# Performance work log

Hardware: AMD Instinct MI355X
Metric: run time of the kernel (lower is better)

Reference implementation:

```python
import jax, jax.numpy as jnp
import numpy as np

B, T = 64, 4096
NUM_CLASSES = 32000
EMBED_DIM = 128


def setup_inputs() -> dict:
    key = jax.random.key(0)
    k_x, k_w, k_b = jax.random.split(key, 3)
    x = jax.random.randint(k_x, (B, T), 0, NUM_CLASSES, dtype=jnp.int64)
    # torch nn.Linear(num_classes, embed_dim): weight (embed_dim, num_classes), bias (embed_dim,)
    W = jax.random.normal(k_w, (EMBED_DIM, NUM_CLASSES), dtype=jnp.float32) * 0.02
    b = jax.random.normal(k_b, (EMBED_DIM,), dtype=jnp.float32) * 0.02
    return {"x": x, "W": W, "b": b}


def reference(x, W, b):
    # one_hot(x) @ W.T + b  ==  gather rows of W.T at x, plus bias
    # W.T: (num_classes, embed_dim); out: (B, T, embed_dim)
    return jnp.take(W.T, x, axis=0) + b
```

## Files before the change

kernel.cpp:

```cpp
#include <hip/hip_runtime.h>

#define NUM_CLASSES 32000
#define EMBED 128
#define NTOK (64 * 4096)
#define CLS_PER_BLK 64
#define NCHUNK (NUM_CLASSES / CLS_PER_BLK)
#define NREP 16
#define SUBCAP 96
#define LDS_STRIDE 132

typedef float f32x4 __attribute__((ext_vector_type(4)));

__global__ __launch_bounds__(256) void bucket_kernel(
    const int* __restrict__ x, int* __restrict__ cnt, int* __restrict__ ids,
    const float* __restrict__ W, const float* __restrict__ bias,
    float* __restrict__ out) {
  const int t = blockIdx.x * 256 + threadIdx.x;
  const int c = x[t];
  const int idx = (c >> 6) * NREP + (blockIdx.x & (NREP - 1));
  const int pos = atomicAdd(&cnt[idx * 16], 1);
  if (pos < SUBCAP) {
    ids[idx * SUBCAP + pos] = ((c & 63) << 18) | t;
  } else {
    for (int e = 0; e < EMBED; ++e)
      out[(size_t)t * EMBED + e] = W[(size_t)e * NUM_CLASSES + c] + bias[e];
  }
}

__global__ __launch_bounds__(512) void fused_gather_kernel(
    const float* __restrict__ W, const float* __restrict__ bias,
    const int* __restrict__ cnt, const int* __restrict__ ids,
    f32x4* __restrict__ out) {
  __shared__ float lds[CLS_PER_BLK * LDS_STRIDE];
  __shared__ int s_ids[NREP * SUBCAP];
  __shared__ int s_cnt[NREP];
  __shared__ int s_ofs[NREP + 1];

  const int chunk = blockIdx.x;
  const int c0 = chunk << 6;
  const int tid = threadIdx.x;

  if (tid < NREP) s_cnt[tid] = min(cnt[(chunk * NREP + tid) * 16], SUBCAP);

  const int tx4 = tid & 15;
  const int ty = tid >> 4;
  for (int e = ty; e < EMBED; e += 32) {
    const f32x4 w = *reinterpret_cast<const f32x4*>(
        W + (size_t)e * NUM_CLASSES + c0 + 4 * tx4);
    const float bv = bias[e];
    lds[(4 * tx4 + 0) * LDS_STRIDE + e] = w.x + bv;
    lds[(4 * tx4 + 1) * LDS_STRIDE + e] = w.y + bv;
    lds[(4 * tx4 + 2) * LDS_STRIDE + e] = w.z + bv;
    lds[(4 * tx4 + 3) * LDS_STRIDE + e] = w.w + bv;
  }
  __syncthreads();

  if (tid == 0) {
    int acc = 0;
    for (int r = 0; r < NREP; ++r) {
      s_ofs[r] = acc;
      acc += s_cnt[r];
    }
    s_ofs[NREP] = acc;
  }
  __syncthreads();

  {
    const int r = tid >> 5;
    const int lane = tid & 31;
    const int nr = s_cnt[r];
    const int o = s_ofs[r];
    const int gbase = (chunk * NREP + r) * SUBCAP;
    for (int i = lane; i < nr; i += 32) s_ids[o + i] = ids[gbase + i];
  }
  __syncthreads();

  const int nTot = s_ofs[NREP];
  const int slot = tid >> 5;
  const int j = tid & 31;
  for (int i = slot; i < nTot; i += 16) {
    const int pk = s_ids[i];
    const int t = pk & 0x3FFFF;
    const int cl = pk >> 18;
    const f32x4 v =
        *reinterpret_cast<const f32x4*>(&lds[cl * LDS_STRIDE + 4 * j]);
    __builtin_nontemporal_store(v, &out[(size_t)t * 32 + j]);
  }
}

__global__ __launch_bounds__(256) void build_table_kernel(
    const float* __restrict__ W, const float* __restrict__ bias,
    float* __restrict__ Wb) {
  __shared__ float lds[EMBED * (CLS_PER_BLK + 1)];
  const int c0 = blockIdx.x * CLS_PER_BLK;
  const int tid = threadIdx.x;
  const int tx = tid & 63;
  const int ty = tid >> 6;
  for (int e = ty; e < EMBED; e += 4) {
    lds[e * (CLS_PER_BLK + 1) + tx] = W[(size_t)e * NUM_CLASSES + c0 + tx];
  }
  __syncthreads();
  const int e = tid & 127;
  const int half = tid >> 7;
  const float bv = bias[e];
  for (int ci = half; ci < CLS_PER_BLK; ci += 2) {
    Wb[(size_t)(c0 + ci) * EMBED + e] = lds[e * (CLS_PER_BLK + 1) + ci] + bv;
  }
}

__global__ __launch_bounds__(256) void gather_kernel(
    const int* __restrict__ x, const float* __restrict__ Wb,
    float* __restrict__ out) {
  const int g = blockIdx.x * 256 + threadIdx.x;
  const int token = g >> 5;
  const int j = g & 31;
  const int c = x[token];
  reinterpret_cast<f32x4*>(out)[g] =
      reinterpret_cast<const f32x4*>(Wb)[(size_t)c * 32 + j];
}

__global__ __launch_bounds__(256) void direct_kernel(
    const int* __restrict__ x, const float* __restrict__ W,
    const float* __restrict__ bias, float* __restrict__ out) {
  const int g = blockIdx.x * 256 + threadIdx.x;
  const int token = g >> 7;
  const int e = g & 127;
  const int c = x[token];
  out[g] = W[(size_t)e * NUM_CLASSES + c] + bias[e];
}

extern "C" void kernel_launch(void* const* d_in, const int* in_sizes, int n_in,
                              void* d_out, int out_size, void* d_ws,
                              size_t ws_size, hipStream_t stream) {
  const int* x = (const int*)d_in[0];
  const float* W = (const float*)d_in[1];
  const float* bias = (const float*)d_in[2];
  float* out = (float*)d_out;

  const size_t cnt_bytes = (size_t)NCHUNK * NREP * 16 * sizeof(int);
  const size_t ids_bytes = (size_t)NCHUNK * NREP * SUBCAP * sizeof(int);
  const size_t need_bucket = cnt_bytes + ids_bytes;
  const size_t table_bytes = (size_t)NUM_CLASSES * EMBED * sizeof(float);

  if (ws_size >= need_bucket) {
    int* cnt = (int*)d_ws;
    int* ids = (int*)((char*)d_ws + cnt_bytes);
    (void)hipMemsetAsync(cnt, 0, cnt_bytes, stream);
    bucket_kernel<<<NTOK / 256, 256, 0, stream>>>(x, cnt, ids, W, bias, out);
    fused_gather_kernel<<<NCHUNK, 512, 0, stream>>>(W, bias, cnt, ids,
                                                    (f32x4*)out);
  } else if (ws_size >= table_bytes) {
    float* Wb = (float*)d_ws;
    build_table_kernel<<<NUM_CLASSES / CLS_PER_BLK, 256, 0, stream>>>(W, bias,
                                                                      Wb);
    gather_kernel<<<(NTOK * 32) / 256, 256, 0, stream>>>(x, Wb, out);
  } else {
    direct_kernel<<<(NTOK * EMBED) / 256, 256, 0, stream>>>(x, W, bias, out);
  }
}
```

Baseline: 174.5 us.

## Vectorize token bucketing and widen fused gather blocks with pipelined LDS reads

The bucketing kernel now reads four token ids per thread with a single vector load and issues four atomics per thread, so it launches a quarter as many blocks. The fused gather kernel doubles its block size to 1024 threads, so the W staging and id copy loops take fewer iterations per thread and 32 token slots run per block. The store loop is software-pipelined: the LDS read for the next token is issued before the nontemporal store of the current one. The aim is to cut launch and per-thread loop overhead and hide LDS latency behind global stores. The cost is that each bucketing thread runs its atomics back to back, and fewer, larger blocks may lower occupancy or balance.

```diff
diff --git a/kernel.cpp b/kernel.cpp
--- a/kernel.cpp
+++ b/kernel.cpp
@@ -10,24 +10,32 @@
 #define LDS_STRIDE 132
 
 typedef float f32x4 __attribute__((ext_vector_type(4)));
+typedef int i32x4 __attribute__((ext_vector_type(4)));
 
 __global__ __launch_bounds__(256) void bucket_kernel(
     const int* __restrict__ x, int* __restrict__ cnt, int* __restrict__ ids,
     const float* __restrict__ W, const float* __restrict__ bias,
     float* __restrict__ out) {
-  const int t = blockIdx.x * 256 + threadIdx.x;
-  const int c = x[t];
-  const int idx = (c >> 6) * NREP + (blockIdx.x & (NREP - 1));
-  const int pos = atomicAdd(&cnt[idx * 16], 1);
-  if (pos < SUBCAP) {
-    ids[idx * SUBCAP + pos] = ((c & 63) << 18) | t;
-  } else {
-    for (int e = 0; e < EMBED; ++e)
-      out[(size_t)t * EMBED + e] = W[(size_t)e * NUM_CLASSES + c] + bias[e];
+  const int g = blockIdx.x * 256 + threadIdx.x;
+  const i32x4 cv = reinterpret_cast<const i32x4*>(x)[g];
+  const int rep = blockIdx.x & (NREP - 1);
+  const int t0 = g * 4;
+#pragma unroll
+  for (int k = 0; k < 4; ++k) {
+    const int c = cv[k];
+    const int t = t0 + k;
+    const int idx = (c >> 6) * NREP + rep;
+    const int pos = atomicAdd(&cnt[idx * 16], 1);
+    if (pos < SUBCAP) {
+      ids[idx * SUBCAP + pos] = ((c & 63) << 18) | t;
+    } else {
+      for (int e = 0; e < EMBED; ++e)
+        out[(size_t)t * EMBED + e] = W[(size_t)e * NUM_CLASSES + c] + bias[e];
+    }
   }
 }
 
-__global__ __launch_bounds__(512) void fused_gather_kernel(
+__global__ __launch_bounds__(1024) void fused_gather_kernel(
     const float* __restrict__ W, const float* __restrict__ bias,
     const int* __restrict__ cnt, const int* __restrict__ ids,
     f32x4* __restrict__ out) {
@@ -44,7 +52,8 @@
 
   const int tx4 = tid & 15;
   const int ty = tid >> 4;
-  for (int e = ty; e < EMBED; e += 32) {
+#pragma unroll
+  for (int e = ty; e < EMBED; e += 64) {
     const f32x4 w = *reinterpret_cast<const f32x4*>(
         W + (size_t)e * NUM_CLASSES + c0 + 4 * tx4);
     const float bv = bias[e];
@@ -66,24 +75,32 @@
   __syncthreads();
 
   {
-    const int r = tid >> 5;
-    const int lane = tid & 31;
+    const int r = tid >> 6;
+    const int lane = tid & 63;
     const int nr = s_cnt[r];
     const int o = s_ofs[r];
     const int gbase = (chunk * NREP + r) * SUBCAP;
-    for (int i = lane; i < nr; i += 32) s_ids[o + i] = ids[gbase + i];
+    for (int i = lane; i < nr; i += 64) s_ids[o + i] = ids[gbase + i];
   }
   __syncthreads();
 
   const int nTot = s_ofs[NREP];
   const int slot = tid >> 5;
   const int j = tid & 31;
-  for (int i = slot; i < nTot; i += 16) {
-    const int pk = s_ids[i];
-    const int t = pk & 0x3FFFF;
-    const int cl = pk >> 18;
-    const f32x4 v =
-        *reinterpret_cast<const f32x4*>(&lds[cl * LDS_STRIDE + 4 * j]);
+  int i = slot;
+  if (i < nTot) {
+    int pk = s_ids[i];
+    f32x4 v = *reinterpret_cast<const f32x4*>(
+        &lds[(pk >> 18) * LDS_STRIDE + 4 * j]);
+    int t = pk & 0x3FFFF;
+    for (i += 32; i < nTot; i += 32) {
+      const int pk1 = s_ids[i];
+      const f32x4 v1 = *reinterpret_cast<const f32x4*>(
+          &lds[(pk1 >> 18) * LDS_STRIDE + 4 * j]);
+      __builtin_nontemporal_store(v, &out[(size_t)t * 32 + j]);
+      v = v1;
+      t = pk1 & 0x3FFFF;
+    }
     __builtin_nontemporal_store(v, &out[(size_t)t * 32 + j]);
   }
 }
@@ -146,9 +163,9 @@
     int* cnt = (int*)d_ws;
     int* ids = (int*)((char*)d_ws + cnt_bytes);
     (void)hipMemsetAsync(cnt, 0, cnt_bytes, stream);
-    bucket_kernel<<<NTOK / 256, 256, 0, stream>>>(x, cnt, ids, W, bias, out);
-    fused_gather_kernel<<<NCHUNK, 512, 0, stream>>>(W, bias, cnt, ids,
-                                                    (f32x4*)out);
+    bucket_kernel<<<NTOK / 1024, 256, 0, stream>>>(x, cnt, ids, W, bias, out);
+    fused_gather_kernel<<<NCHUNK, 1024, 0, stream>>>(W, bias, cnt, ids,
+                                                     (f32x4*)out);
   } else if (ws_size >= table_bytes) {
     float* Wb = (float*)d_ws;
     build_table_kernel<<<NUM_CLASSES / CLS_PER_BLK, 256, 0, stream>>>(W, bias,
```

Measured after the change: 174.8 us. About the same (+0.2%).

## Fuse memset, bucketing and gather into one cooperative kernel with grid syncs

Applied to the files above, without the earlier changes.

Replaces the memset plus the bucket and gather kernel launches with a single cooperative kernel. It stages the W chunk into LDS, zeroes the counters, grid-syncs, buckets tokens with a grid-stride loop, grid-syncs again, then scatters rows from LDS. The goal is to remove launch gaps and overlap the W staging with bucketing. It adds two grid-wide barriers and needs all 500 blocks of 512 threads resident at once; if the cooperative launch fails, the old two-kernel path runs. The gather loop is also software-pipelined so the next LDS read overlaps the current store, and the table-based fallback path is removed.

```diff
diff --git a/kernel.cpp b/kernel.cpp
--- a/kernel.cpp
+++ b/kernel.cpp
@@ -1,4 +1,7 @@
 #include <hip/hip_runtime.h>
+#include <hip/hip_cooperative_groups.h>
+
+namespace cg = cooperative_groups;
 
 #define NUM_CLASSES 32000
 #define EMBED 128
@@ -8,8 +11,102 @@
 #define NREP 16
 #define SUBCAP 96
 #define LDS_STRIDE 132
+#define FUSED_THREADS 512
 
 typedef float f32x4 __attribute__((ext_vector_type(4)));
+
+__global__ __launch_bounds__(FUSED_THREADS) void fused_all_kernel(
+    const int* __restrict__ x, const float* __restrict__ W,
+    const float* __restrict__ bias, int* __restrict__ cnt,
+    int* __restrict__ ids, f32x4* __restrict__ out) {
+  __shared__ float lds[CLS_PER_BLK * LDS_STRIDE];
+  __shared__ int s_ids[NREP * SUBCAP];
+  __shared__ int s_cnt[NREP];
+  __shared__ int s_ofs[NREP + 1];
+
+  const int chunk = blockIdx.x;
+  const int c0 = chunk << 6;
+  const int tid = threadIdx.x;
+  cg::grid_group grid = cg::this_grid();
+
+  {
+    const int tx4 = tid & 15;
+    const int ty = tid >> 4;
+#pragma unroll
+    for (int e = ty; e < EMBED; e += 32) {
+      const f32x4 w = *reinterpret_cast<const f32x4*>(
+          W + (size_t)e * NUM_CLASSES + c0 + 4 * tx4);
+      const float bv = bias[e];
+      lds[(4 * tx4 + 0) * LDS_STRIDE + e] = w.x + bv;
+      lds[(4 * tx4 + 1) * LDS_STRIDE + e] = w.y + bv;
+      lds[(4 * tx4 + 2) * LDS_STRIDE + e] = w.z + bv;
+      lds[(4 * tx4 + 3) * LDS_STRIDE + e] = w.w + bv;
+    }
+    for (int i = tid; i < NREP * 16; i += FUSED_THREADS)
+      __hip_atomic_store(&cnt[chunk * NREP * 16 + i], 0, __ATOMIC_RELAXED,
+                         __HIP_MEMORY_SCOPE_AGENT);
+  }
+  grid.sync();
+
+  {
+    const int gsize = NCHUNK * FUSED_THREADS;
+    const int rep = blockIdx.x & (NREP - 1);
+    for (int t = blockIdx.x * FUSED_THREADS + tid; t < NTOK; t += gsize) {
+      const int c = x[t];
+      const int idx = (c >> 6) * NREP + rep;
+      const int pos = atomicAdd(&cnt[idx * 16], 1);
+      if (pos < SUBCAP) {
+        ids[idx * SUBCAP + pos] = ((c & 63) << 18) | t;
+      } else {
+        for (int e = 0; e < EMBED; ++e)
+          out[((size_t)t * EMBED + e) >> 2][e & 3] =
+              W[(size_t)e * NUM_CLASSES + c] + bias[e];
+      }
+    }
+  }
+  grid.sync();
+
+  if (tid < NREP) s_cnt[tid] = min(cnt[(chunk * NREP + tid) * 16], SUBCAP);
+  __syncthreads();
+  if (tid == 0) {
+    int acc = 0;
+    for (int r = 0; r < NREP; ++r) {
+      s_ofs[r] = acc;
+      acc += s_cnt[r];
+    }
+    s_ofs[NREP] = acc;
+  }
+  __syncthreads();
+  {
+    const int r = tid >> 5;
+    const int lane = tid & 31;
+    const int nr = s_cnt[r];
+    const int o = s_ofs[r];
+    const int gbase = (chunk * NREP + r) * SUBCAP;
+    for (int i = lane; i < nr; i += 32) s_ids[o + i] = ids[gbase + i];
+  }
+  __syncthreads();
+
+  const int nTot = s_ofs[NREP];
+  const int slot = tid >> 5;
+  const int j = tid & 31;
+  int i = slot;
+  if (i < nTot) {
+    int pk = s_ids[i];
+    f32x4 v =
+        *reinterpret_cast<const f32x4*>(&lds[(pk >> 18) * LDS_STRIDE + 4 * j]);
+    int t = pk & 0x3FFFF;
+    for (i += 16; i < nTot; i += 16) {
+      const int pk1 = s_ids[i];
+      const f32x4 v1 = *reinterpret_cast<const f32x4*>(
+          &lds[(pk1 >> 18) * LDS_STRIDE + 4 * j]);
+      __builtin_nontemporal_store(v, &out[(size_t)t * 32 + j]);
+      v = v1;
+      t = pk1 & 0x3FFFF;
+    }
+    __builtin_nontemporal_store(v, &out[(size_t)t * 32 + j]);
+  }
+}
 
 __global__ __launch_bounds__(256) void bucket_kernel(
     const int* __restrict__ x, int* __restrict__ cnt, int* __restrict__ ids,
@@ -35,15 +132,13 @@
   __shared__ int s_ids[NREP * SUBCAP];
   __shared__ int s_cnt[NREP];
   __shared__ int s_ofs[NREP + 1];
-
   const int chunk = blockIdx.x;
   const int c0 = chunk << 6;
   const int tid = threadIdx.x;
-
   if (tid < NREP) s_cnt[tid] = min(cnt[(chunk * NREP + tid) * 16], SUBCAP);
-
   const int tx4 = tid & 15;
   const int ty = tid >> 4;
+#pragma unroll
   for (int e = ty; e < EMBED; e += 32) {
     const f32x4 w = *reinterpret_cast<const f32x4*>(
         W + (size_t)e * NUM_CLASSES + c0 + 4 * tx4);
@@ -54,7 +149,6 @@
     lds[(4 * tx4 + 3) * LDS_STRIDE + e] = w.w + bv;
   }
   __syncthreads();
-
   if (tid == 0) {
     int acc = 0;
     for (int r = 0; r < NREP; ++r) {
@@ -64,7 +158,6 @@
     s_ofs[NREP] = acc;
   }
   __syncthreads();
-
   {
     const int r = tid >> 5;
     const int lane = tid & 31;
@@ -74,49 +167,25 @@
     for (int i = lane; i < nr; i += 32) s_ids[o + i] = ids[gbase + i];
   }
   __syncthreads();
-
   const int nTot = s_ofs[NREP];
   const int slot = tid >> 5;
   const int j = tid & 31;
-  for (int i = slot; i < nTot; i += 16) {
-    const int pk = s_ids[i];
-    const int t = pk & 0x3FFFF;
-    const int cl = pk >> 18;
-    const f32x4 v =
-        *reinterpret_cast<const f32x4*>(&lds[cl * LDS_STRIDE + 4 * j]);
+  int i = slot;
+  if (i < nTot) {
+    int pk = s_ids[i];
+    f32x4 v =
+        *reinterpret_cast<const f32x4*>(&lds[(pk >> 18) * LDS_STRIDE + 4 * j]);
+    int t = pk & 0x3FFFF;
+    for (i += 16; i < nTot; i += 16) {
+      const int pk1 = s_ids[i];
+      const f32x4 v1 = *reinterpret_cast<const f32x4*>(
+          &lds[(pk1 >> 18) * LDS_STRIDE + 4 * j]);
+      __builtin_nontemporal_store(v, &out[(size_t)t * 32 + j]);
+      v = v1;
+      t = pk1 & 0x3FFFF;
+    }
     __builtin_nontemporal_store(v, &out[(size_t)t * 32 + j]);
   }
-}
-
-__global__ __launch_bounds__(256) void build_table_kernel(
-    const float* __restrict__ W, const float* __restrict__ bias,
-    float* __restrict__ Wb) {
-  __shared__ float lds[EMBED * (CLS_PER_BLK + 1)];
-  const int c0 = blockIdx.x * CLS_PER_BLK;
-  const int tid = threadIdx.x;
-  const int tx = tid & 63;
-  const int ty = tid >> 6;
-  for (int e = ty; e < EMBED; e += 4) {
-    lds[e * (CLS_PER_BLK + 1) + tx] = W[(size_t)e * NUM_CLASSES + c0 + tx];
-  }
-  __syncthreads();
-  const int e = tid & 127;
-  const int half = tid >> 7;
-  const float bv = bias[e];
-  for (int ci = half; ci < CLS_PER_BLK; ci += 2) {
-    Wb[(size_t)(c0 + ci) * EMBED + e] = lds[e * (CLS_PER_BLK + 1) + ci] + bv;
-  }
-}
-
-__global__ __launch_bounds__(256) void gather_kernel(
-    const int* __restrict__ x, const float* __restrict__ Wb,
-    float* __restrict__ out) {
-  const int g = blockIdx.x * 256 + threadIdx.x;
-  const int token = g >> 5;
-  const int j = g & 31;
-  const int c = x[token];
-  reinterpret_cast<f32x4*>(out)[g] =
-      reinterpret_cast<const f32x4*>(Wb)[(size_t)c * 32 + j];
 }
 
 __global__ __launch_bounds__(256) void direct_kernel(
@@ -140,20 +209,27 @@
   const size_t cnt_bytes = (size_t)NCHUNK * NREP * 16 * sizeof(int);
   const size_t ids_bytes = (size_t)NCHUNK * NREP * SUBCAP * sizeof(int);
   const size_t need_bucket = cnt_bytes + ids_bytes;
-  const size_t table_bytes = (size_t)NUM_CLASSES * EMBED * sizeof(float);
 
   if (ws_size >= need_bucket) {
     int* cnt = (int*)d_ws;
     int* ids = (int*)((char*)d_ws + cnt_bytes);
+    f32x4* out4 = (f32x4*)out;
+
+    const int* x_ = x;
+    const float* W_ = W;
+    const float* b_ = bias;
+    int* cnt_ = cnt;
+    int* ids_ = ids;
+    f32x4* out_ = out4;
+    void* args[] = {&x_, &W_, &b_, &cnt_, &ids_, &out_};
+    hipError_t err = hipLaunchCooperativeKernel(
+        (const void*)fused_all_kernel, dim3(NCHUNK), dim3(FUSED_THREADS), args,
+        0, stream);
+    if (err == hipSuccess) return;
+
     (void)hipMemsetAsync(cnt, 0, cnt_bytes, stream);
     bucket_kernel<<<NTOK / 256, 256, 0, stream>>>(x, cnt, ids, W, bias, out);
-    fused_gather_kernel<<<NCHUNK, 512, 0, stream>>>(W, bias, cnt, ids,
-                                                    (f32x4*)out);
-  } else if (ws_size >= table_bytes) {
-    float* Wb = (float*)d_ws;
-    build_table_kernel<<<NUM_CLASSES / CLS_PER_BLK, 256, 0, stream>>>(W, bias,
-                                                                      Wb);
-    gather_kernel<<<(NTOK * 32) / 256, 256, 0, stream>>>(x, Wb, out);
+    fused_gather_kernel<<<NCHUNK, 512, 0, stream>>>(W, bias, cnt, ids, out4);
   } else {
     direct_kernel<<<(NTOK * EMBED) / 256, 256, 0, stream>>>(x, W, bias, out);
   }
```

New measurement: 307.8 us. 76.4% more time.
